# Kernel tuning notes

Hardware: AMD Instinct MI355X
Metric: run time of the kernel (lower is better)

## Reference

```python
import jax, jax.numpy as jnp
import numpy as np

B, T, D, H = 4, 2048, 1024, 16
HD = D // H  # 64
NEG = -np.finfo(np.float32).max


def setup_inputs() -> dict:
    key = jax.random.key(0)
    ks = jax.random.split(key, 9)
    s = 1.0 / np.sqrt(D)
    return {
        "x": jax.random.normal(ks[0], (B, T, D), jnp.float32),
        "wq": jax.random.normal(ks[1], (D, D), jnp.float32) * s,
        "bq": jax.random.normal(ks[2], (D,), jnp.float32) * 0.02,
        "wk": jax.random.normal(ks[3], (D, D), jnp.float32) * s,
        "bk": jax.random.normal(ks[4], (D,), jnp.float32) * 0.02,
        "wv": jax.random.normal(ks[5], (D, D), jnp.float32) * s,
        "bv": jax.random.normal(ks[6], (D,), jnp.float32) * 0.02,
        "wo": jax.random.normal(ks[7], (D, D), jnp.float32) * s,
        "bo": jax.random.normal(ks[8], (D,), jnp.float32) * 0.02,
    }


def reference(x, wq, bq, wk, bk, wv, bv, wo, bo):
    b, t, d = x.shape
    # separate Q, K, V projections, reshape to (B, H, T, HD)
    def proj(w, bias):
        y = x @ w + bias
        return y.reshape(b, t, H, HD).transpose(0, 2, 1, 3)
    q = proj(wq, bq)
    k = proj(wk, bk)
    v = proj(wv, bv)
    scale = 1.0 / np.sqrt(HD).astype(np.float32)
    scores = jnp.einsum("bhqd,bhkd->bhqk", q, k) * scale  # (B,H,T,T)
    # causal mask: -max_float on strictly upper triangle (matches source)
    mask = jnp.triu(jnp.full((t, t), NEG, jnp.float32), k=1)
    attn = jax.nn.softmax(scores + mask, axis=-1)
    out = jnp.einsum("bhqk,bhkd->bhqd", attn, v)
    out = out.transpose(0, 2, 1, 3).reshape(b, t, d)
    return out @ wo + bo
```

## Files before the change

kernel.cpp:

```cpp
#include <hip/hip_runtime.h>

typedef __bf16 bf16x8 __attribute__((ext_vector_type(8)));
typedef float f32x4 __attribute__((ext_vector_type(4)));

#define B_ 4
#define T_ 2048
#define D_ 1024
#define H_ 16
#define HD_ 64
#define M_ 8192
#define QSCALE 0.1803368801111204f

__device__ __forceinline__ ushort f2b(float f) {
  union { float f; unsigned u; } v; v.f = f;
  unsigned u = v.u;
  return (ushort)((u + 0x7FFFu + ((u >> 16) & 1u)) >> 16);
}

__device__ __forceinline__ unsigned pkbf(float a, float b) {
  union { float f; unsigned u; } va, vb; va.f = a; vb.f = b;
  return __builtin_amdgcn_perm(vb.u + 0x8000u, va.u + 0x8000u, 0x07060302u);
}

__device__ __forceinline__ void gll16(const void* g, void* l) {
  __builtin_amdgcn_global_load_lds(
      (const __attribute__((address_space(1))) unsigned*)g,
      (__attribute__((address_space(3))) unsigned*)l, 16, 0, 0);
}

__global__ __launch_bounds__(256) void cast_x_kernel(const float* __restrict__ x,
                                                     ushort* __restrict__ xb) {
  int idx = blockIdx.x * 256 + threadIdx.x;
  float4 v = ((const float4*)x)[idx];
  ushort4 o;
  o.x = f2b(v.x); o.y = f2b(v.y); o.z = f2b(v.z); o.w = f2b(v.w);
  ((ushort4*)xb)[idx] = o;
}

__global__ __launch_bounds__(256) void transpose_w_kernel(
    const float* __restrict__ wq, const float* __restrict__ wk,
    const float* __restrict__ wv, const float* __restrict__ wo,
    ushort* __restrict__ wt_qkv, ushort* __restrict__ wt_o) {
  __shared__ float tile[32][33];
  int z = blockIdx.z;
  const float* src = (z == 0) ? wq : (z == 1) ? wk : (z == 2) ? wv : wo;
  ushort* dst = (z < 3) ? (wt_qkv + (size_t)z * D_ * D_) : wt_o;
  int n0 = blockIdx.x * 32, k0 = blockIdx.y * 32;
  int tx = threadIdx.x & 31, ty = threadIdx.x >> 5;
  for (int i = 0; i < 4; i++) {
    int r = ty + i * 8;
    tile[r][tx] = src[(size_t)(k0 + r) * D_ + n0 + tx];
  }
  __syncthreads();
  for (int i = 0; i < 4; i++) {
    int r = ty + i * 8;
    dst[(size_t)(n0 + r) * D_ + k0 + tx] = f2b(tile[tx][r]);
  }
}

__global__ __launch_bounds__(256) void gemm_kernel(
    const ushort* __restrict__ A, const ushort* __restrict__ Bt, int mode,
    const float* __restrict__ bias_q, const float* __restrict__ bias_k,
    const float* __restrict__ bias_v,
    ushort* __restrict__ qb, ushort* __restrict__ kb, ushort* __restrict__ vtb,
    float* __restrict__ outf) {
  __shared__ ushort As[2][128][64];
  __shared__ ushort Bs[2][128][64];
  int tid = threadIdx.x;
  int wave = tid >> 6, lane = tid & 63, lrow = lane >> 4, lcol = lane & 15;

  int gx = gridDim.x;
  int nwg = gx * gridDim.y;
  int orig = blockIdx.x + gx * blockIdx.y;
  int work = (orig & 7) * (nwg >> 3) + (orig >> 3);
  int m0 = (work / gx) * 128, n0 = (work % gx) * 128;
  int wm = (wave & 1) * 64, wn = (wave >> 1) * 64;

  int rb = tid >> 3;
  int dc = tid & 7;
  int scv = dc ^ (rb & 7);
  const ushort* aBase = A + (size_t)(m0 + rb) * D_ + scv * 8;
  const ushort* bBase = Bt + (size_t)(n0 + rb) * D_ + scv * 8;

  f32x4 zero = {0.f, 0.f, 0.f, 0.f};
  f32x4 acc[4][4];
  for (int i = 0; i < 4; i++)
    for (int j = 0; j < 4; j++) acc[i][j] = zero;

  int swz = lcol & 7;

  auto stage = [&](int buf, int k) {
#pragma unroll
    for (int g = 0; g < 4; g++) {
      gll16(aBase + (size_t)(32 * g) * D_ + k, &As[buf][0][0] + tid * 8 + g * 2048);
      gll16(bBase + (size_t)(32 * g) * D_ + k, &Bs[buf][0][0] + tid * 8 + g * 2048);
    }
  };

  stage(0, 0);

  for (int k0 = 0; k0 < D_; k0 += 64) {
    int cur = (k0 >> 6) & 1, nxt = cur ^ 1;
    __syncthreads();
    if (k0 + 64 < D_) stage(nxt, k0 + 64);

    for (int ks = 0; ks < 2; ks++) {
      bf16x8 af[4], bf[4];
      int ch = ((ks * 4 + lrow) ^ swz) * 8;
      for (int mt = 0; mt < 4; mt++)
        af[mt] = *(const bf16x8*)&As[cur][wm + mt * 16 + lcol][ch];
      for (int nt = 0; nt < 4; nt++)
        bf[nt] = *(const bf16x8*)&Bs[cur][wn + nt * 16 + lcol][ch];
      for (int mt = 0; mt < 4; mt++)
        for (int nt = 0; nt < 4; nt++)
          acc[mt][nt] = __builtin_amdgcn_mfma_f32_16x16x32_bf16(
              af[mt], bf[nt], acc[mt][nt], 0, 0, 0);
    }
  }

  if (mode == 0) {
    int proj = n0 >> 10;
    const float* bias = (proj == 0) ? bias_q : (proj == 1) ? bias_k : bias_v;
    for (int mt = 0; mt < 4; mt++) {
      int gm0 = m0 + wm + mt * 16 + lrow * 4;
      int b = gm0 >> 11, tp = gm0 & 2047;
      for (int nt = 0; nt < 4; nt++) {
        int gn = n0 + wn + nt * 16 + lcol;
        int inner = gn & 1023;
        int h = inner >> 6, hd = inner & 63;
        float bv = bias[inner];
        if (proj == 0) {
          size_t base = ((size_t)(b * H_ + h) * T_ + tp) * HD_ + hd;
          for (int r = 0; r < 4; r++)
            qb[base + (size_t)r * HD_] = f2b((acc[mt][nt][r] + bv) * QSCALE);
        } else if (proj == 1) {
          size_t base = ((size_t)(b * H_ + h) * T_ + tp) * HD_ + hd;
          for (int r = 0; r < 4; r++)
            kb[base + (size_t)r * HD_] = f2b(acc[mt][nt][r] + bv);
        } else {
          ushort4 pk;
          pk.x = f2b(acc[mt][nt][0] + bv);
          pk.y = f2b(acc[mt][nt][1] + bv);
          pk.z = f2b(acc[mt][nt][2] + bv);
          pk.w = f2b(acc[mt][nt][3] + bv);
          *(ushort4*)&vtb[((size_t)(b * H_ + h) * HD_ + hd) * T_ + tp] = pk;
        }
      }
    }
  } else {
    for (int mt = 0; mt < 4; mt++) {
      int gm0 = m0 + wm + mt * 16 + lrow * 4;
      for (int nt = 0; nt < 4; nt++) {
        int gn = n0 + wn + nt * 16 + lcol;
        float bv = bias_q[gn];
        for (int r = 0; r < 4; r++)
          outf[(size_t)(gm0 + r) * D_ + gn] = acc[mt][nt][r] + bv;
      }
    }
  }
}

__global__ __launch_bounds__(256) void flash_kernel(
    const ushort* __restrict__ qb, const ushort* __restrict__ kb,
    const ushort* __restrict__ vtb, ushort* __restrict__ ob) {
  __shared__ ushort Ks[64][80];
  __shared__ ushort Vs[64][80];
  __shared__ ushort Ps[4][32][80];
  int tid = threadIdx.x;
  int wave = tid >> 6, lane = tid & 63, lrow = lane >> 4, lcol = lane & 15;

  int bid = blockIdx.x + (blockIdx.y << 4);
  int xcd = bid & 7;
  int slot = bid >> 3;
  int bh = xcd * 8 + (slot >> 4);
  int qblk = 15 - (slot & 15);
  int b = bh >> 4, h = bh & 15;
  const ushort* qp = qb + (size_t)bh * T_ * HD_;
  const ushort* kh = kb + (size_t)bh * T_ * HD_;
  const ushort* vh = vtb + (size_t)bh * HD_ * T_;

  int r0 = tid >> 3, cb0 = (tid & 7) * 8;
  uint4 kr0 = *(const uint4*)&kh[(size_t)r0 * HD_ + cb0];
  uint4 kr1 = *(const uint4*)&kh[(size_t)(r0 + 32) * HD_ + cb0];
  uint4 vr0 = *(const uint4*)&vh[(size_t)r0 * T_ + cb0];
  uint4 vr1 = *(const uint4*)&vh[(size_t)(r0 + 32) * T_ + cb0];

  bf16x8 af1;
  {
    __bf16 ov = (__bf16)((lcol == 0) ? 1.0f : 0.0f);
    for (int i = 0; i < 8; i++) af1[i] = ov;
  }

  f32x4 zero = {0.f, 0.f, 0.f, 0.f};

  int q0w = qblk * 128 + wave * 32;
  bf16x8 qf[2][2];
#pragma unroll
  for (int qh = 0; qh < 2; qh++)
#pragma unroll
    for (int ks = 0; ks < 2; ks++)
      qf[qh][ks] = *(const bf16x8*)&qp[(size_t)(q0w + qh * 16 + lcol) * HD_ +
                                       ks * 32 + lrow * 8];

  f32x4 accO[2][4];
  f32x4 accS[2];
#pragma unroll
  for (int qh = 0; qh < 2; qh++) {
    accS[qh] = zero;
    for (int mt = 0; mt < 4; mt++) accO[qh][mt] = zero;
  }

  int nj = qblk * 2 + 2;
  for (int j = 0; j < nj; j++) {
    __syncthreads();
    *(uint4*)&Ks[r0][cb0] = kr0;
    *(uint4*)&Ks[r0 + 32][cb0] = kr1;
    *(uint4*)&Vs[r0][cb0] = vr0;
    *(uint4*)&Vs[r0 + 32][cb0] = vr1;
    __syncthreads();

    if (j + 1 < nj) {
      int jn = j + 1;
      kr0 = *(const uint4*)&kh[(size_t)(jn * 64 + r0) * HD_ + cb0];
      kr1 = *(const uint4*)&kh[(size_t)(jn * 64 + r0 + 32) * HD_ + cb0];
      vr0 = *(const uint4*)&vh[(size_t)r0 * T_ + jn * 64 + cb0];
      vr1 = *(const uint4*)&vh[(size_t)(r0 + 32) * T_ + jn * 64 + cb0];
    }

    if (j * 64 > q0w + 31) continue;

    f32x4 st[2][4];
#pragma unroll
    for (int qh = 0; qh < 2; qh++)
      for (int mt = 0; mt < 4; mt++) st[qh][mt] = zero;
    __builtin_amdgcn_s_setprio(1);
#pragma unroll
    for (int ks = 0; ks < 2; ks++)
#pragma unroll
      for (int mt = 0; mt < 4; mt++) {
        bf16x8 kf = *(const bf16x8*)&Ks[mt * 16 + lcol][ks * 32 + lrow * 8];
        st[0][mt] = __builtin_amdgcn_mfma_f32_16x16x32_bf16(kf, qf[0][ks], st[0][mt], 0, 0, 0);
        st[1][mt] = __builtin_amdgcn_mfma_f32_16x16x32_bf16(kf, qf[1][ks], st[1][mt], 0, 0, 0);
      }
    __builtin_amdgcn_s_setprio(0);

    if (j >= 2 * qblk) {
#pragma unroll
      for (int qh = 0; qh < 2; qh++) {
        int q_g = q0w + qh * 16 + lcol;
#pragma unroll
        for (int mt = 0; mt < 4; mt++)
          for (int r = 0; r < 4; r++) {
            int kv_g = j * 64 + mt * 16 + lrow * 4 + r;
            if (kv_g > q_g) st[qh][mt][r] = -1e30f;
          }
      }
    }

#pragma unroll
    for (int qh = 0; qh < 2; qh++)
      for (int mt = 0; mt < 4; mt++)
        for (int r = 0; r < 4; r++)
          st[qh][mt][r] = __builtin_amdgcn_exp2f(st[qh][mt][r]);

#pragma unroll
    for (int qh = 0; qh < 2; qh++)
      for (int mt = 0; mt < 4; mt++) {
        uint2 pk;
        pk.x = pkbf(st[qh][mt][0], st[qh][mt][1]);
        pk.y = pkbf(st[qh][mt][2], st[qh][mt][3]);
        *(uint2*)&Ps[wave][qh * 16 + lcol][mt * 16 + lrow * 4] = pk;
      }

    __builtin_amdgcn_s_setprio(1);
#pragma unroll
    for (int ks = 0; ks < 2; ks++) {
      bf16x8 pf0 = *(const bf16x8*)&Ps[wave][lcol][ks * 32 + lrow * 8];
      bf16x8 pf1 = *(const bf16x8*)&Ps[wave][16 + lcol][ks * 32 + lrow * 8];
      accS[0] = __builtin_amdgcn_mfma_f32_16x16x32_bf16(af1, pf0, accS[0], 0, 0, 0);
      accS[1] = __builtin_amdgcn_mfma_f32_16x16x32_bf16(af1, pf1, accS[1], 0, 0, 0);
#pragma unroll
      for (int mt = 0; mt < 4; mt++) {
        bf16x8 vf = *(const bf16x8*)&Vs[mt * 16 + lcol][ks * 32 + lrow * 8];
        accO[0][mt] = __builtin_amdgcn_mfma_f32_16x16x32_bf16(vf, pf0, accO[0][mt], 0, 0, 0);
        accO[1][mt] = __builtin_amdgcn_mfma_f32_16x16x32_bf16(vf, pf1, accO[1][mt], 0, 0, 0);
      }
    }
    __builtin_amdgcn_s_setprio(0);
  }

#pragma unroll
  for (int qh = 0; qh < 2; qh++) {
    float lsum = __shfl(accS[qh][0], lcol);
    float linv = 1.f / lsum;
    int t = q0w + qh * 16 + lcol;
    size_t base = ((size_t)b * T_ + t) * D_ + h * HD_;
#pragma unroll
    for (int mt = 0; mt < 4; mt++) {
      uint2 pk;
      pk.x = pkbf(accO[qh][mt][0] * linv, accO[qh][mt][1] * linv);
      pk.y = pkbf(accO[qh][mt][2] * linv, accO[qh][mt][3] * linv);
      *(uint2*)&ob[base + mt * 16 + lrow * 4] = pk;
    }
  }
}

extern "C" void kernel_launch(void* const* d_in, const int* in_sizes, int n_in,
                              void* d_out, int out_size, void* d_ws, size_t ws_size,
                              hipStream_t stream) {
  (void)in_sizes; (void)n_in; (void)out_size; (void)ws_size;
  const float* x  = (const float*)d_in[0];
  const float* wq = (const float*)d_in[1];
  const float* bq = (const float*)d_in[2];
  const float* wk = (const float*)d_in[3];
  const float* bk = (const float*)d_in[4];
  const float* wv = (const float*)d_in[5];
  const float* bv = (const float*)d_in[6];
  const float* wo = (const float*)d_in[7];
  const float* bo = (const float*)d_in[8];
  float* out = (float*)d_out;

  char* ws = (char*)d_ws;
  ushort* xb     = (ushort*)(ws);
  ushort* wt_qkv = (ushort*)(ws + 16777216);
  ushort* wt_o   = (ushort*)(ws + 23068672);
  ushort* qb     = (ushort*)(ws + 25165824);
  ushort* kb     = (ushort*)(ws + 41943040);
  ushort* vtb    = (ushort*)(ws + 58720256);
  ushort* ob     = (ushort*)(ws + 75497472);

  cast_x_kernel<<<8192, 256, 0, stream>>>(x, xb);
  transpose_w_kernel<<<dim3(32, 32, 4), 256, 0, stream>>>(wq, wk, wv, wo, wt_qkv, wt_o);
  gemm_kernel<<<dim3(24, 64), 256, 0, stream>>>(xb, wt_qkv, 0, bq, bk, bv, qb, kb, vtb, nullptr);
  flash_kernel<<<dim3(16, 64), 256, 0, stream>>>(qb, kb, vtb, ob);
  gemm_kernel<<<dim3(8, 64), 256, 0, stream>>>(ob, wt_o, 1, bo, nullptr, nullptr,
                                               nullptr, nullptr, nullptr, out);
}
```

Baseline: 270.4 us.

## Pair causal query blocks per workgroup and double-buffer swizzled K/V tiles

Each flash workgroup now handles two query blocks (15-p and p), so every block does the same total causal work. This halves the grid and removes the tail imbalance. K/V staging moves to a double-buffered LDS ring with one barrier per tile, prefetching two tiles ahead. The padded LDS rows are replaced by an XOR swizzle, including for the P tile. The trade-off is fewer workgroups, which may hurt occupancy and latency hiding, and higher register pressure from holding two sets of Q fragments.

After: 247.0 us. 1.1x faster.

```diff
diff --git a/kernel.cpp b/kernel.cpp
--- a/kernel.cpp
+++ b/kernel.cpp
@@ -163,146 +163,173 @@
 __global__ __launch_bounds__(256) void flash_kernel(
     const ushort* __restrict__ qb, const ushort* __restrict__ kb,
     const ushort* __restrict__ vtb, ushort* __restrict__ ob) {
-  __shared__ ushort Ks[64][80];
-  __shared__ ushort Vs[64][80];
-  __shared__ ushort Ps[4][32][80];
+  __shared__ ushort Ks2[2][64][64];
+  __shared__ ushort Vs2[2][64][64];
+  __shared__ ushort Ps[4][32][64];
   int tid = threadIdx.x;
   int wave = tid >> 6, lane = tid & 63, lrow = lane >> 4, lcol = lane & 15;
 
-  int bid = blockIdx.x + (blockIdx.y << 4);
+  int bid = blockIdx.x + (blockIdx.y << 3);
   int xcd = bid & 7;
   int slot = bid >> 3;
-  int bh = xcd * 8 + (slot >> 4);
-  int qblk = 15 - (slot & 15);
+  int bh = xcd * 8 + (slot >> 3);
+  int p = slot & 7;
+  int qb0 = 15 - p, qb1 = p;
   int b = bh >> 4, h = bh & 15;
   const ushort* qp = qb + (size_t)bh * T_ * HD_;
   const ushort* kh = kb + (size_t)bh * T_ * HD_;
   const ushort* vh = vtb + (size_t)bh * HD_ * T_;
 
-  int r0 = tid >> 3, cb0 = (tid & 7) * 8;
-  uint4 kr0 = *(const uint4*)&kh[(size_t)r0 * HD_ + cb0];
-  uint4 kr1 = *(const uint4*)&kh[(size_t)(r0 + 32) * HD_ + cb0];
-  uint4 vr0 = *(const uint4*)&vh[(size_t)r0 * T_ + cb0];
-  uint4 vr1 = *(const uint4*)&vh[(size_t)(r0 + 32) * T_ + cb0];
+  int n0 = 2 * qb0 + 2;
+  int ntot = n0 + 2 * qb1 + 2;
+
+  int r0 = tid >> 3, dc = tid & 7;
+  int wsl = (dc ^ (r0 & 7)) * 8;
+  int rsw = lcol & 7;
+
+  uint4 kr0, kr1, vr0, vr1;
+  auto gload = [&](int jt) {
+    kr0 = *(const uint4*)&kh[(size_t)(jt * 64 + r0) * HD_ + dc * 8];
+    kr1 = *(const uint4*)&kh[(size_t)(jt * 64 + r0 + 32) * HD_ + dc * 8];
+    vr0 = *(const uint4*)&vh[(size_t)r0 * T_ + jt * 64 + dc * 8];
+    vr1 = *(const uint4*)&vh[(size_t)(r0 + 32) * T_ + jt * 64 + dc * 8];
+  };
+  auto swrite = [&](int buf) {
+    *(uint4*)&Ks2[buf][r0][wsl] = kr0;
+    *(uint4*)&Ks2[buf][r0 + 32][wsl] = kr1;
+    *(uint4*)&Vs2[buf][r0][wsl] = vr0;
+    *(uint4*)&Vs2[buf][r0 + 32][wsl] = vr1;
+  };
 
   bf16x8 af1;
   {
     __bf16 ov = (__bf16)((lcol == 0) ? 1.0f : 0.0f);
-    for (int i = 0; i < 8; i++) af1[i] = ov;
+    for (int i2 = 0; i2 < 8; i2++) af1[i2] = ov;
   }
 
   f32x4 zero = {0.f, 0.f, 0.f, 0.f};
 
-  int q0w = qblk * 128 + wave * 32;
-  bf16x8 qf[2][2];
+  gload(0);
+  swrite(0);
+  gload(1);
+  __syncthreads();
+
+  int q0wA = qb0 * 128 + wave * 32, q0wB = qb1 * 128 + wave * 32;
+  bf16x8 qfA[2][2], qfB[2][2];
 #pragma unroll
   for (int qh = 0; qh < 2; qh++)
 #pragma unroll
-    for (int ks = 0; ks < 2; ks++)
-      qf[qh][ks] = *(const bf16x8*)&qp[(size_t)(q0w + qh * 16 + lcol) * HD_ +
-                                       ks * 32 + lrow * 8];
-
-  f32x4 accO[2][4];
-  f32x4 accS[2];
-#pragma unroll
-  for (int qh = 0; qh < 2; qh++) {
-    accS[qh] = zero;
-    for (int mt = 0; mt < 4; mt++) accO[qh][mt] = zero;
-  }
-
-  int nj = qblk * 2 + 2;
-  for (int j = 0; j < nj; j++) {
-    __syncthreads();
-    *(uint4*)&Ks[r0][cb0] = kr0;
-    *(uint4*)&Ks[r0 + 32][cb0] = kr1;
-    *(uint4*)&Vs[r0][cb0] = vr0;
-    *(uint4*)&Vs[r0 + 32][cb0] = vr1;
-    __syncthreads();
-
-    if (j + 1 < nj) {
-      int jn = j + 1;
-      kr0 = *(const uint4*)&kh[(size_t)(jn * 64 + r0) * HD_ + cb0];
-      kr1 = *(const uint4*)&kh[(size_t)(jn * 64 + r0 + 32) * HD_ + cb0];
-      vr0 = *(const uint4*)&vh[(size_t)r0 * T_ + jn * 64 + cb0];
-      vr1 = *(const uint4*)&vh[(size_t)(r0 + 32) * T_ + jn * 64 + cb0];
-    }
-
-    if (j * 64 > q0w + 31) continue;
-
-    f32x4 st[2][4];
-#pragma unroll
-    for (int qh = 0; qh < 2; qh++)
-      for (int mt = 0; mt < 4; mt++) st[qh][mt] = zero;
-    __builtin_amdgcn_s_setprio(1);
-#pragma unroll
-    for (int ks = 0; ks < 2; ks++)
-#pragma unroll
-      for (int mt = 0; mt < 4; mt++) {
-        bf16x8 kf = *(const bf16x8*)&Ks[mt * 16 + lcol][ks * 32 + lrow * 8];
-        st[0][mt] = __builtin_amdgcn_mfma_f32_16x16x32_bf16(kf, qf[0][ks], st[0][mt], 0, 0, 0);
-        st[1][mt] = __builtin_amdgcn_mfma_f32_16x16x32_bf16(kf, qf[1][ks], st[1][mt], 0, 0, 0);
-      }
-    __builtin_amdgcn_s_setprio(0);
-
-    if (j >= 2 * qblk) {
-#pragma unroll
-      for (int qh = 0; qh < 2; qh++) {
-        int q_g = q0w + qh * 16 + lcol;
-#pragma unroll
-        for (int mt = 0; mt < 4; mt++)
-          for (int r = 0; r < 4; r++) {
-            int kv_g = j * 64 + mt * 16 + lrow * 4 + r;
-            if (kv_g > q_g) st[qh][mt][r] = -1e30f;
+    for (int ks = 0; ks < 2; ks++) {
+      qfA[qh][ks] = *(const bf16x8*)&qp[(size_t)(q0wA + qh * 16 + lcol) * HD_ +
+                                        ks * 32 + lrow * 8];
+      qfB[qh][ks] = *(const bf16x8*)&qp[(size_t)(q0wB + qh * 16 + lcol) * HD_ +
+                                        ks * 32 + lrow * 8];
+    }
+
+  auto run_pass = [&](int qblk, int q0w, int base, const bf16x8 qf[2][2]) {
+    f32x4 accO[2][4];
+    f32x4 accS[2];
+#pragma unroll
+    for (int qh = 0; qh < 2; qh++) {
+      accS[qh] = zero;
+      for (int mt = 0; mt < 4; mt++) accO[qh][mt] = zero;
+    }
+
+    int nj = 2 * qblk + 2;
+    for (int j = 0; j < nj; j++) {
+      int g = base + j, cur = g & 1;
+      bool active = (j * 64 <= q0w + 31);
+
+      if (active) {
+        f32x4 st[2][4];
+#pragma unroll
+        for (int qh = 0; qh < 2; qh++)
+          for (int mt = 0; mt < 4; mt++) st[qh][mt] = zero;
+        __builtin_amdgcn_s_setprio(1);
+#pragma unroll
+        for (int ks = 0; ks < 2; ks++)
+#pragma unroll
+          for (int mt = 0; mt < 4; mt++) {
+            bf16x8 kf = *(const bf16x8*)&Ks2[cur][mt * 16 + lcol]
+                                            [((ks * 4 + lrow) ^ rsw) * 8];
+            st[0][mt] = __builtin_amdgcn_mfma_f32_16x16x32_bf16(kf, qf[0][ks], st[0][mt], 0, 0, 0);
+            st[1][mt] = __builtin_amdgcn_mfma_f32_16x16x32_bf16(kf, qf[1][ks], st[1][mt], 0, 0, 0);
           }
-      }
-    }
-
-#pragma unroll
-    for (int qh = 0; qh < 2; qh++)
-      for (int mt = 0; mt < 4; mt++)
-        for (int r = 0; r < 4; r++)
-          st[qh][mt][r] = __builtin_amdgcn_exp2f(st[qh][mt][r]);
-
-#pragma unroll
-    for (int qh = 0; qh < 2; qh++)
+        __builtin_amdgcn_s_setprio(0);
+
+        if (j >= 2 * qblk) {
+#pragma unroll
+          for (int qh = 0; qh < 2; qh++) {
+            int q_g = q0w + qh * 16 + lcol;
+#pragma unroll
+            for (int mt = 0; mt < 4; mt++)
+              for (int r = 0; r < 4; r++) {
+                int kv_g = j * 64 + mt * 16 + lrow * 4 + r;
+                if (kv_g > q_g) st[qh][mt][r] = -1e30f;
+              }
+          }
+        }
+
+#pragma unroll
+        for (int qh = 0; qh < 2; qh++)
+          for (int mt = 0; mt < 4; mt++)
+            for (int r = 0; r < 4; r++)
+              st[qh][mt][r] = __builtin_amdgcn_exp2f(st[qh][mt][r]);
+
+#pragma unroll
+        for (int qh = 0; qh < 2; qh++)
+          for (int mt = 0; mt < 4; mt++) {
+            uint2 pk;
+            pk.x = pkbf(st[qh][mt][0], st[qh][mt][1]);
+            pk.y = pkbf(st[qh][mt][2], st[qh][mt][3]);
+            int sl = ((2 * mt + (lrow >> 1)) ^ rsw) * 8 + (lrow & 1) * 4;
+            *(uint2*)&Ps[wave][qh * 16 + lcol][sl] = pk;
+          }
+
+        __builtin_amdgcn_s_setprio(1);
+#pragma unroll
+        for (int ks = 0; ks < 2; ks++) {
+          int ch = ((ks * 4 + lrow) ^ rsw) * 8;
+          bf16x8 pf0 = *(const bf16x8*)&Ps[wave][lcol][ch];
+          bf16x8 pf1 = *(const bf16x8*)&Ps[wave][16 + lcol][ch];
+          accS[0] = __builtin_amdgcn_mfma_f32_16x16x32_bf16(af1, pf0, accS[0], 0, 0, 0);
+          accS[1] = __builtin_amdgcn_mfma_f32_16x16x32_bf16(af1, pf1, accS[1], 0, 0, 0);
+#pragma unroll
+          for (int mt = 0; mt < 4; mt++) {
+            bf16x8 vf = *(const bf16x8*)&Vs2[cur][mt * 16 + lcol][ch];
+            accO[0][mt] = __builtin_amdgcn_mfma_f32_16x16x32_bf16(vf, pf0, accO[0][mt], 0, 0, 0);
+            accO[1][mt] = __builtin_amdgcn_mfma_f32_16x16x32_bf16(vf, pf1, accO[1][mt], 0, 0, 0);
+          }
+        }
+        __builtin_amdgcn_s_setprio(0);
+      }
+
+      if (g + 1 < ntot) swrite(cur ^ 1);
+      if (g + 2 < ntot) {
+        int s = g + 2;
+        gload(s < n0 ? s : s - n0);
+      }
+      __syncthreads();
+    }
+
+#pragma unroll
+    for (int qh = 0; qh < 2; qh++) {
+      float lsum = __shfl(accS[qh][0], lcol);
+      float linv = 1.f / lsum;
+      int t = q0w + qh * 16 + lcol;
+      size_t base2 = ((size_t)b * T_ + t) * D_ + h * HD_;
+#pragma unroll
       for (int mt = 0; mt < 4; mt++) {
         uint2 pk;
-        pk.x = pkbf(st[qh][mt][0], st[qh][mt][1]);
-        pk.y = pkbf(st[qh][mt][2], st[qh][mt][3]);
-        *(uint2*)&Ps[wave][qh * 16 + lcol][mt * 16 + lrow * 4] = pk;
-      }
-
-    __builtin_amdgcn_s_setprio(1);
-#pragma unroll
-    for (int ks = 0; ks < 2; ks++) {
-      bf16x8 pf0 = *(const bf16x8*)&Ps[wave][lcol][ks * 32 + lrow * 8];
-      bf16x8 pf1 = *(const bf16x8*)&Ps[wave][16 + lcol][ks * 32 + lrow * 8];
-      accS[0] = __builtin_amdgcn_mfma_f32_16x16x32_bf16(af1, pf0, accS[0], 0, 0, 0);
-      accS[1] = __builtin_amdgcn_mfma_f32_16x16x32_bf16(af1, pf1, accS[1], 0, 0, 0);
-#pragma unroll
-      for (int mt = 0; mt < 4; mt++) {
-        bf16x8 vf = *(const bf16x8*)&Vs[mt * 16 + lcol][ks * 32 + lrow * 8];
-        accO[0][mt] = __builtin_amdgcn_mfma_f32_16x16x32_bf16(vf, pf0, accO[0][mt], 0, 0, 0);
-        accO[1][mt] = __builtin_amdgcn_mfma_f32_16x16x32_bf16(vf, pf1, accO[1][mt], 0, 0, 0);
-      }
-    }
-    __builtin_amdgcn_s_setprio(0);
-  }
-
-#pragma unroll
-  for (int qh = 0; qh < 2; qh++) {
-    float lsum = __shfl(accS[qh][0], lcol);
-    float linv = 1.f / lsum;
-    int t = q0w + qh * 16 + lcol;
-    size_t base = ((size_t)b * T_ + t) * D_ + h * HD_;
-#pragma unroll
-    for (int mt = 0; mt < 4; mt++) {
-      uint2 pk;
-      pk.x = pkbf(accO[qh][mt][0] * linv, accO[qh][mt][1] * linv);
-      pk.y = pkbf(accO[qh][mt][2] * linv, accO[qh][mt][3] * linv);
-      *(uint2*)&ob[base + mt * 16 + lrow * 4] = pk;
-    }
-  }
+        pk.x = pkbf(accO[qh][mt][0] * linv, accO[qh][mt][1] * linv);
+        pk.y = pkbf(accO[qh][mt][2] * linv, accO[qh][mt][3] * linv);
+        *(uint2*)&ob[base2 + mt * 16 + lrow * 4] = pk;
+      }
+    }
+  };
+
+  run_pass(qb0, q0wA, 0, qfA);
+  run_pass(qb1, q0wB, n0, qfB);
 }
 
 extern "C" void kernel_launch(void* const* d_in, const int* in_sizes, int n_in,
@@ -332,7 +359,7 @@
   cast_x_kernel<<<8192, 256, 0, stream>>>(x, xb);
   transpose_w_kernel<<<dim3(32, 32, 4), 256, 0, stream>>>(wq, wk, wv, wo, wt_qkv, wt_o);
   gemm_kernel<<<dim3(24, 64), 256, 0, stream>>>(xb, wt_qkv, 0, bq, bk, bv, qb, kb, vtb, nullptr);
-  flash_kernel<<<dim3(16, 64), 256, 0, stream>>>(qb, kb, vtb, ob);
+  flash_kernel<<<dim3(8, 64), 256, 0, stream>>>(qb, kb, vtb, ob);
   gemm_kernel<<<dim3(8, 64), 256, 0, stream>>>(ob, wt_o, 1, bo, nullptr, nullptr,
                                                nullptr, nullptr, nullptr, out);
 }
```
